# Optimization experiments

Measured on AMD Instinct MI355X. Metric: run time of the kernel, lower is better.

## Reference

```python
import jax, jax.numpy as jnp
import numpy as np

B, L, H, TE = 256, 2048, 64, 64  # batch, seq len, hidden_size, num_time_enc_dims


def _lin_init(k, out_d, in_d):
    bound = 1.0 / np.sqrt(in_d)
    kw, kb = jax.random.split(k)
    w = jax.random.uniform(kw, (out_d, in_d), jnp.float32, -bound, bound)
    b = jax.random.uniform(kb, (out_d,), jnp.float32, -bound, bound)
    return w, b


def setup_inputs() -> dict:
    key = jax.random.key(0)
    ks = jax.random.split(key, 16)
    x_xy = jax.random.normal(ks[0], (B, L, 2), jnp.float32)
    mask = jax.random.bernoulli(ks[1], 0.8, (B, L, 1)).astype(jnp.float32)  # 0 => masked position
    x = jnp.concatenate([x_xy, mask], axis=-1)  # (B,L,3)
    t = jax.random.uniform(ks[2], (B, L, 1), jnp.float32)
    te_w1, te_b1 = _lin_init(ks[3], TE, 1)
    te_w2, te_b2 = _lin_init(ks[4], TE, TE)
    fproj_w, fproj_b = _lin_init(ks[5], H, 3 + TE)
    bproj_w, bproj_b = _lin_init(ks[6], H, 3 + TE)
    fwz, fbz = _lin_init(ks[7], H, H)
    fwh, fbh = _lin_init(ks[8], H, H)
    bwz, bbz = _lin_init(ks[9], H, H)
    bwh, bbh = _lin_init(ks[10], H, H)
    head_hidden = max((2 * H + TE) // 2, 128)  # = 128
    gh_w1, gh_b1 = _lin_init(ks[11], head_hidden, 2 * H + TE)
    gh_w2, gh_b2 = _lin_init(ks[12], 1, head_hidden)
    mask_token = jnp.array([0.0, 0.01], jnp.float32) + jnp.array([0.1, 0.001], jnp.float32) * jax.random.normal(ks[13], (2,), jnp.float32)
    return dict(x=x, t=t, mask_token=mask_token,
                te_w1=te_w1, te_b1=te_b1, te_w2=te_w2, te_b2=te_b2,
                fproj_w=fproj_w, fproj_b=fproj_b, bproj_w=bproj_w, bproj_b=bproj_b,
                fwz=fwz, fbz=fbz, fwh=fwh, fbh=fbh,
                bwz=bwz, bbz=bbz, bwh=bwh, bbh=bbh,
                gh_w1=gh_w1, gh_b1=gh_b1, gh_w2=gh_w2, gh_b2=gh_b2)


def _mingru_prestates(inp, wz, bz, wh, bh, reverse):
    # inp: (B,L,H). Returns the hidden state BEFORE each step's update, in
    # time order, matching the torch code which stores h_* before cell.step.
    z = jax.nn.sigmoid(jnp.einsum('blh,oh->blo', inp, wz) + bz)
    h_tilde = jnp.tanh(jnp.einsum('blh,oh->blo', inp, wh) + bh)

    def step(h, zh):
        z_t, ht_t = zh
        return (1.0 - z_t) * h + z_t * ht_t, h  # emit pre-update carry

    h0 = jnp.zeros((inp.shape[0], wz.shape[0]), inp.dtype)
    _, hs = jax.lax.scan(step, h0,
                         (jnp.swapaxes(z, 0, 1), jnp.swapaxes(h_tilde, 0, 1)),
                         reverse=reverse)
    return jnp.swapaxes(hs, 0, 1)  # (B,L,H)


def reference(x, t, mask_token,
              te_w1, te_b1, te_w2, te_b2,
              fproj_w, fproj_b, bproj_w, bproj_b,
              fwz, fbz, fwh, fbh,
              bwz, bbz, bwh, bbh,
              gh_w1, gh_b1, gh_w2, gh_b2):
    mask_chan = x[..., 2:3]                      # (B,L,1)
    masked_pos = mask_chan == 0
    x_first2 = jnp.where(masked_pos, mask_token.reshape(1, 1, 2), x[..., :2])
    x3 = jnp.concatenate([x_first2, mask_chan], axis=-1)  # (B,L,3)

    t_enc = jax.nn.relu(jnp.einsum('blk,ok->blo', t, te_w1) + te_b1)
    t_enc = jnp.einsum('blk,ok->blo', t_enc, te_w2) + te_b2  # (B,L,TE)

    x_cat = jnp.concatenate([x3, t_enc], axis=-1)  # (B,L,3+TE)

    inp_fwd = jnp.einsum('blk,ok->blo', x_cat, fproj_w) + fproj_b
    inp_bwd = jnp.einsum('blk,ok->blo', x_cat, bproj_w) + bproj_b

    h_fwd = _mingru_prestates(inp_fwd, fwz, fbz, fwh, fbh, reverse=False)  # state after steps 0..t-1
    h_bwd = _mingru_prestates(inp_bwd, bwz, bbz, bwh, bbh, reverse=True)   # state after steps L-1..t+1

    h_fwd_final = h_fwd[:, -1:, :]  # state after steps 0..L-2
    h_bwd_final = h_bwd[:, 0:1, :]  # state after steps L-1..1

    unmasked = mask_chan > 0
    h_fwd_apply = jnp.where(unmasked, h_fwd, h_fwd_final)
    h_bwd_apply = jnp.where(unmasked, h_bwd, h_bwd_final)

    h_bi = jnp.concatenate([h_fwd_apply, h_bwd_apply, t_enc], axis=-1)  # (B,L,2H+TE)
    hid = jax.nn.relu(jnp.einsum('blk,ok->blo', h_bi, gh_w1) + gh_b1)
    preds = jnp.einsum('blk,ok->blo', hid, gh_w2) + gh_b2  # (B,L,1)
    return preds
```

## Files before the change

kernel.cpp:

```cpp
#include <hip/hip_runtime.h>
#include <stdint.h>

#define NB 256
#define NL 2048

typedef __attribute__((ext_vector_type(8))) short short8;
typedef __attribute__((ext_vector_type(4))) float f32x4;
#define MFMA16(a,b,c) __builtin_amdgcn_mfma_f32_16x16x32_bf16(a,b,c,0,0,0)

static __device__ __forceinline__ unsigned short f2bf(float f) {
    union { float f; uint32_t u; } v; v.f = f;
    uint32_t u = v.u;
    uint32_t r = u + 0x7fffu + ((u >> 16) & 1u);
    return (unsigned short)(r >> 16);
}
static __device__ __forceinline__ float bflo(uint32_t u) {
    union { uint32_t u; float f; } v; v.u = u << 16; return v.f;
}
static __device__ __forceinline__ float bfhi(uint32_t u) {
    union { uint32_t u; float f; } v; v.u = u & 0xffff0000u; return v.f;
}
#if __has_builtin(__builtin_amdgcn_cvt_pk_bf16_f32)
typedef __attribute__((ext_vector_type(2))) __bf16 bf16x2_t;
static __device__ __forceinline__ uint32_t pk2(float lo, float hi) {
    union { bf16x2_t v; uint32_t u; } c;
    c.v = __builtin_amdgcn_cvt_pk_bf16_f32(lo, hi);
    return c.u;
}
static __device__ __forceinline__ unsigned short bf1(float v) {
    union { bf16x2_t v; uint32_t u; } c;
    c.v = __builtin_amdgcn_cvt_pk_bf16_f32(v, v);
    return (unsigned short)(c.u & 0xffffu);
}
#else
static __device__ __forceinline__ uint32_t pk2(float lo, float hi) {
    return ((uint32_t)f2bf(hi) << 16) | (uint32_t)f2bf(lo);
}
static __device__ __forceinline__ unsigned short bf1(float v) { return f2bf(v); }
#endif
static __device__ __forceinline__ short8 frag8(const float* p) {
    short8 r;
#pragma unroll
    for (int j = 0; j < 8; ++j) r[j] = (short)f2bf(p[j]);
    return r;
}

static __device__ __forceinline__ void barrier_lds() {
    asm volatile("s_waitcnt lgkmcnt(0)" ::: "memory");
    __builtin_amdgcn_s_barrier();
}

#define SSTR 129

__global__ __launch_bounds__(512) void scan_fused(
    const float* __restrict__ x, const float* __restrict__ t,
    const float* __restrict__ mtok,
    const float* __restrict__ te_w1, const float* __restrict__ te_b1,
    const float* __restrict__ te_w2, const float* __restrict__ te_b2,
    const float* __restrict__ fpw, const float* __restrict__ fpb,
    const float* __restrict__ bpw, const float* __restrict__ bpb,
    const float* __restrict__ fwz, const float* __restrict__ fbz,
    const float* __restrict__ fwh, const float* __restrict__ fbh,
    const float* __restrict__ bwz, const float* __restrict__ bbz,
    const float* __restrict__ bwh, const float* __restrict__ bbh,
    int b0,
    unsigned short* __restrict__ hf, unsigned short* __restrict__ hb)
{
    __shared__ __align__(16) unsigned short s_tenc[128*72];
    __shared__ __align__(16) unsigned short s_inp[128*72];
    __shared__ uint32_t s_seg[64*SSTR];
    __shared__ float s_A[8][65], s_B[8][65];
    __shared__ float s_H[64];
    __shared__ float2 s_wb[64];

    const int rl  = blockIdx.x >> 1;
    const int dir = blockIdx.x & 1;
    const int tid = threadIdx.x;
    const int h   = tid & 63;
    const int q   = tid >> 6;
    const int lq  = h >> 4;
    const int ln  = h & 15;
    const int mq  = q >> 1;
    const int nh  = q & 1;

    const int gx = (b0 + rl) << 11;
    unsigned short* out = (dir ? hb : hf) + (size_t)rl * NL * 64;

    short8 bte[2][2];
    float bite[2];
#pragma unroll
    for (int ni = 0; ni < 2; ++ni) {
        const int nt = nh*2 + ni;
        const float* row = te_w2 + (nt*16 + ln)*64;
#pragma unroll
        for (int ks = 0; ks < 2; ++ks) bte[ni][ks] = frag8(row + lq*8 + ks*32);
        bite[ni] = te_b2[nt*16 + ln];
    }
    const float* PW = dir ? bpw : fpw;
    const float* PB = dir ? bpb : fpb;
    short8 bpj[2][3];
    float bipj[2];
#pragma unroll
    for (int ni = 0; ni < 2; ++ni) {
        const int nt = nh*2 + ni;
        const float* row = PW + (nt*16 + ln)*67;
#pragma unroll
        for (int ks = 0; ks < 2; ++ks) {
            float tmp[8];
#pragma unroll
            for (int j = 0; j < 8; ++j) tmp[j] = row[3 + lq*8 + ks*32 + j];
            bpj[ni][ks] = frag8(tmp);
        }
        {
            float tmp[8];
#pragma unroll
            for (int j = 0; j < 8; ++j) tmp[j] = (lq == 0 && j < 3) ? row[j] : 0.f;
            bpj[ni][2] = frag8(tmp);
        }
        bipj[ni] = PB[nt*16 + ln];
    }
    const float* WZ = dir ? bwz : fwz;
    const float* WH = dir ? bwh : fwh;
    const float* BZ = dir ? bbz : fbz;
    const float* BH = dir ? bbh : fbh;
    short8 bz[2][2], bh[2][2];
    float biz[2], bih[2];
#pragma unroll
    for (int ni = 0; ni < 2; ++ni) {
        const int nt = nh*2 + ni;
        const float* rz = WZ + (nt*16 + ln)*64;
        const float* rh = WH + (nt*16 + ln)*64;
#pragma unroll
        for (int ks = 0; ks < 2; ++ks) {
            bz[ni][ks] = frag8(rz + lq*8 + ks*32);
            bh[ni][ks] = frag8(rh + lq*8 + ks*32);
        }
        biz[ni] = BZ[nt*16 + ln];
        bih[ni] = BH[nt*16 + ln];
    }
    const float mt0 = mtok[0], mt1 = mtok[1];

    auto G1 = [&](const float* tvv) {
#pragma unroll
        for (int mi = 0; mi < 2; ++mi) {
            short8 a0, a1;
#pragma unroll
            for (int j = 0; j < 8; ++j) {
                const float2 wb0 = s_wb[lq*8 + j];
                const float2 wb1 = s_wb[lq*8 + 32 + j];
                a0[j] = (short)bf1(fmaxf(fmaf(tvv[mi], wb0.x, wb0.y), 0.f));
                a1[j] = (short)bf1(fmaxf(fmaf(tvv[mi], wb1.x, wb1.y), 0.f));
            }
#pragma unroll
            for (int ni = 0; ni < 2; ++ni) {
                f32x4 c = {0.f, 0.f, 0.f, 0.f};
                c = MFMA16(a0, bte[ni][0], c);
                c = MFMA16(a1, bte[ni][1], c);
                const int o = (nh*2+ni)*16 + ln;
#pragma unroll
                for (int r = 0; r < 4; ++r)
                    s_tenc[((mq*2+mi)*16 + lq*4 + r)*72 + o] = bf1(c[r] + bite[ni]);
            }
        }
    };
    auto G2 = [&](const float* xr0_, const float* xr1_, const float* xmc_) {
#pragma unroll
        for (int mi = 0; mi < 2; ++mi) {
            const int mrow = (mq*2+mi)*16 + ln;
            const short8 a0 = *(const short8*)(s_tenc + mrow*72 + lq*8);
            const short8 a1 = *(const short8*)(s_tenc + mrow*72 + lq*8 + 32);
            short8 a2 = {0,0,0,0,0,0,0,0};
            if (lq == 0) {
                const float mc  = xmc_[mi];
                const float x0m = (mc == 0.f) ? mt0 : xr0_[mi];
                const float x1m = (mc == 0.f) ? mt1 : xr1_[mi];
                a2[0] = (short)bf1(x0m);
                a2[1] = (short)bf1(x1m);
                a2[2] = (short)bf1(mc);
            }
#pragma unroll
            for (int ni = 0; ni < 2; ++ni) {
                f32x4 c = {0.f, 0.f, 0.f, 0.f};
                c = MFMA16(a0, bpj[ni][0], c);
                c = MFMA16(a1, bpj[ni][1], c);
                c = MFMA16(a2, bpj[ni][2], c);
                const int o = (nh*2+ni)*16 + ln;
#pragma unroll
                for (int r = 0; r < 4; ++r)
                    s_inp[((mq*2+mi)*16 + lq*4 + r)*72 + o] = bf1(c[r] + bipj[ni]);
            }
        }
    };
    auto GATES = [&]() {
#pragma unroll
        for (int mi = 0; mi < 2; ++mi) {
            const int mrow = (mq*2+mi)*16 + ln;
            const short8 a0 = *(const short8*)(s_inp + mrow*72 + lq*8);
            const short8 a1 = *(const short8*)(s_inp + mrow*72 + lq*8 + 32);
#pragma unroll
            for (int ni = 0; ni < 2; ++ni) {
                f32x4 cz  = {0.f, 0.f, 0.f, 0.f};
                f32x4 ch2 = {0.f, 0.f, 0.f, 0.f};
                cz  = MFMA16(a0, bz[ni][0], cz);
                cz  = MFMA16(a1, bz[ni][1], cz);
                ch2 = MFMA16(a0, bh[ni][0], ch2);
                ch2 = MFMA16(a1, bh[ni][1], ch2);
                const int hcol = (nh*2+ni)*16 + ln;
#pragma unroll
                for (int r = 0; r < 4; ++r) {
                    const float az = cz[r]  + biz[ni];
                    const float ah = ch2[r] + bih[ni];
                    const float z  = __builtin_amdgcn_rcpf(1.f + __expf(-az));
                    const float cc = fminf(fmaxf(ah, -15.f), 15.f);
                    const float e2 = __expf(2.f * cc);
                    const float th = 1.f - 2.f * __builtin_amdgcn_rcpf(e2 + 1.f);
                    s_seg[hcol*SSTR + (mq*2+mi)*16 + lq*4 + r] = pk2(1.f - z, z * th);
                }
            }
        }
    };

    if (tid < 64) {
        s_H[tid] = 0.f;
        s_wb[tid] = make_float2(te_w1[tid], te_b1[tid]);
    }
    barrier_lds();

    const int s0 = dir ? 15 : 0;
    {
        float tv0[2];
#pragma unroll
        for (int mi = 0; mi < 2; ++mi)
            tv0[mi] = t[gx + s0*128 + (mq*2+mi)*16 + ln];
        G1(tv0);
    }
    barrier_lds();
    {
        float xr0_[2], xr1_[2], xmc_[2];
        if (lq == 0) {
#pragma unroll
            for (int mi = 0; mi < 2; ++mi) {
                const float* xp = x + (size_t)(gx + s0*128 + (mq*2+mi)*16 + ln)*3;
                xr0_[mi] = xp[0]; xr1_[mi] = xp[1]; xmc_[mi] = xp[2];
            }
        }
        G2(xr0_, xr1_, xmc_);
    }
    barrier_lds();

    uint32_t regs[16];
    int l0p = 0;

#pragma unroll 1
    for (int si = 0; si < 16; ++si) {
        const int s = dir ? (15 - si) : si;
        const int sn = dir ? (14 - si) : (si + 1);
        if (si > 0) {
            float hv = s_A[q][h];
#pragma unroll
            for (int i = 0; i < 16; ++i) {
                const int g = q*16 + i;
                const int xx = dir ? (127 - g) : g;
                out[(size_t)(l0p + xx)*64 + h] = bf1(hv);
                hv = fmaf(bflo(regs[i]), hv, bfhi(regs[i]));
            }
        }
        GATES();
        barrier_lds();
        float tvn[2];
        if (si < 15) {
#pragma unroll
            for (int mi = 0; mi < 2; ++mi)
                tvn[mi] = t[gx + sn*128 + (mq*2+mi)*16 + ln];
        }
        {
            float A = 1.f, Bc = 0.f;
#pragma unroll
            for (int i = 0; i < 16; ++i) {
                const int g = q*16 + i;
                const int xx = dir ? (127 - g) : g;
                const uint32_t uab = s_seg[h*SSTR + xx];
                regs[i] = uab;
                Bc = fmaf(bflo(uab), Bc, bfhi(uab));
                A *= bflo(uab);
            }
            s_A[q][h] = A; s_B[q][h] = Bc;
        }
        if (si < 15) G1(tvn);
        barrier_lds();
        float xr0_[2], xr1_[2], xmc_[2];
        if (si < 15 && lq == 0) {
#pragma unroll
            for (int mi = 0; mi < 2; ++mi) {
                const float* xp = x + (size_t)(gx + sn*128 + (mq*2+mi)*16 + ln)*3;
                xr0_[mi] = xp[0]; xr1_[mi] = xp[1]; xmc_[mi] = xp[2];
            }
        }
        if (tid < 64) {
            float H = s_H[tid];
#pragma unroll
            for (int qq = 0; qq < 8; ++qq) {
                const float a = s_A[qq][tid], b = s_B[qq][tid];
                s_A[qq][tid] = H;
                H = fmaf(a, H, b);
            }
            s_H[tid] = H;
        }
        if (si < 15) G2(xr0_, xr1_, xmc_);
        barrier_lds();
        l0p = s * 128;
    }
    {
        float hv = s_A[q][h];
#pragma unroll
        for (int i = 0; i < 16; ++i) {
            const int g = q*16 + i;
            const int xx = dir ? (127 - g) : g;
            out[(size_t)(l0p + xx)*64 + h] = bf1(hv);
            hv = fmaf(bflo(regs[i]), hv, bfhi(regs[i]));
        }
    }
}

__global__ __launch_bounds__(256, 3) void head_kernel(
    const float* __restrict__ x, const float* __restrict__ t,
    const float* __restrict__ te_w1, const float* __restrict__ te_b1,
    const float* __restrict__ te_w2, const float* __restrict__ te_b2,
    const unsigned short* __restrict__ hf, const unsigned short* __restrict__ hb,
    const float* __restrict__ w1, const float* __restrict__ b1,
    const float* __restrict__ w2, const float* __restrict__ b2,
    int b0,
    float* __restrict__ out)
{
    __shared__ __align__(16) unsigned short s_a[64*200];
    __shared__ float s_part[4][64];
    __shared__ float s_mcall[256];
    __shared__ float2 s_wb[64];

    const int tid = threadIdx.x;
    const int w   = tid >> 6;
    const int l   = tid & 63;
    const int lq  = l >> 4;
    const int ln  = l & 15;

    short8 bw1[2][6];
    float b1v[2], w2v[2];
#pragma unroll
    for (int p = 0; p < 2; ++p) {
        const int o = (2*w + p)*16 + ln;
        const float* row = w1 + o*192;
#pragma unroll
        for (int ks = 0; ks < 6; ++ks) bw1[p][ks] = frag8(row + lq*8 + ks*32);
        b1v[p] = b1[o];
        w2v[p] = w2[o];
    }
    short8 bte[2];
    {
        const float* row = te_w2 + (w*16 + ln)*64;
#pragma unroll
        for (int ks = 0; ks < 2; ++ks) bte[ks] = frag8(row + lq*8 + ks*32);
    }
    const float bias_te = te_b2[w*16 + ln];
    const float bias2 = b2[0];

    const int baseposl = blockIdx.x * 256;
    const int gbase0 = (b0 << 11) + baseposl;

    uint4 greg[4];

    auto GISSUE = [&](int ch) {
        const int chbase = baseposl + ch*64;
        const int ll0 = chbase & 2047;
        const int bl  = chbase >> 11;
        const size_t rowbase = (size_t)bl * NL * 64;
#pragma unroll
        for (int rep = 0; rep < 4; ++rep) {
            const int idx = rep*256 + tid;
            const int seg = idx >> 9;
            const int row = (idx >> 3) & 63;
            const int c   = idx & 7;
            const bool unm = s_mcall[ch*64 + row] > 0.f;
            const uint4* src = (seg == 0)
                ? (const uint4*)(hf + rowbase + (size_t)(unm ? (ll0+row) : (NL-1))*64)
                : (const uint4*)(hb + rowbase + (size_t)(unm ? (ll0+row) : 0)*64);
            greg[rep] = src[c];
        }
    };
    auto GWRITE = [&]() {
#pragma unroll
        for (int rep = 0; rep < 4; ++rep) {
            const int idx = rep*256 + tid;
            const int seg = idx >> 9;
            const int row = (idx >> 3) & 63;
            const int c   = idx & 7;
            ((uint4*)s_a)[row*25 + seg*8 + c] = greg[rep];
        }
    };
    auto TENC = [&](int ch) {
        const int chbase = gbase0 + ch*64;
        const int o = w*16 + ln;
#pragma unroll
        for (int mt = 0; mt < 4; ++mt) {
            const float tv = t[chbase + mt*16 + ln];
            short8 a0, a1;
#pragma unroll
            for (int j = 0; j < 8; ++j) {
                const float2 wb0 = s_wb[lq*8 + j];
                const float2 wb1 = s_wb[lq*8 + 32 + j];
                a0[j] = (short)bf1(fmaxf(fmaf(tv, wb0.x, wb0.y), 0.f));
                a1[j] = (short)bf1(fmaxf(fmaf(tv, wb1.x, wb1.y), 0.f));
            }
            f32x4 c = {0.f, 0.f, 0.f, 0.f};
            c = MFMA16(a0, bte[0], c);
            c = MFMA16(a1, bte[1], c);
#pragma unroll
            for (int r = 0; r < 4; ++r)
                s_a[(mt*16 + lq*4 + r)*200 + 128 + o] = bf1(c[r] + bias_te);
        }
    };
    auto Cp = [&]() {
#pragma unroll
        for (int mt = 0; mt < 4; ++mt) {
            short8 af[6];
#pragma unroll
            for (int ks = 0; ks < 6; ++ks)
                af[ks] = *(const short8*)(s_a + (mt*16+ln)*200 + lq*8 + ks*32);
            float vs[4] = {0.f, 0.f, 0.f, 0.f};
#pragma unroll
            for (int p = 0; p < 2; ++p) {
                f32x4 c = {0.f, 0.f, 0.f, 0.f};
#pragma unroll
                for (int ks = 0; ks < 6; ++ks) c = MFMA16(af[ks], bw1[p][ks], c);
#pragma unroll
                for (int r = 0; r < 4; ++r)
                    vs[r] += fmaxf(c[r] + b1v[p], 0.f) * w2v[p];
            }
#pragma unroll
            for (int mask = 1; mask < 16; mask <<= 1) {
#pragma unroll
                for (int r = 0; r < 4; ++r)
                    vs[r] += __shfl_xor(vs[r], mask);
            }
            if (ln == 0) {
#pragma unroll
                for (int r = 0; r < 4; ++r)
                    s_part[w][mt*16 + lq*4 + r] = vs[r];
            }
        }
    };
    auto Dp = [&](int ch) {
        if (tid < 64) {
            out[gbase0 + ch*64 + tid] = s_part[0][tid] + s_part[1][tid]
                                      + s_part[2][tid] + s_part[3][tid] + bias2;
        }
    };

    s_mcall[tid] = x[(size_t)(gbase0 + tid)*3 + 2];
    if (tid < 64) s_wb[tid] = make_float2(te_w1[tid], te_b1[tid]);
    barrier_lds();
    GISSUE(0);

#pragma unroll 1
    for (int ch = 0; ch < 4; ++ch) {
        if (ch > 0) Dp(ch - 1);
        TENC(ch);
        GWRITE();
        barrier_lds();
        if (ch < 3) GISSUE(ch + 1);
        Cp();
        barrier_lds();
    }
    Dp(3);
}

extern "C" void kernel_launch(void* const* d_in, const int* in_sizes, int n_in,
                              void* d_out, int out_size, void* d_ws, size_t ws_size,
                              hipStream_t stream)
{
    const float* x     = (const float*)d_in[0];
    const float* t     = (const float*)d_in[1];
    const float* mtok  = (const float*)d_in[2];
    const float* te_w1 = (const float*)d_in[3];
    const float* te_b1 = (const float*)d_in[4];
    const float* te_w2 = (const float*)d_in[5];
    const float* te_b2 = (const float*)d_in[6];
    const float* fpw   = (const float*)d_in[7];
    const float* fpb   = (const float*)d_in[8];
    const float* bpw   = (const float*)d_in[9];
    const float* bpb   = (const float*)d_in[10];
    const float* fwz   = (const float*)d_in[11];
    const float* fbz   = (const float*)d_in[12];
    const float* fwh   = (const float*)d_in[13];
    const float* fbh   = (const float*)d_in[14];
    const float* bwz   = (const float*)d_in[15];
    const float* bbz   = (const float*)d_in[16];
    const float* bwh   = (const float*)d_in[17];
    const float* bbh   = (const float*)d_in[18];
    const float* w1    = (const float*)d_in[19];
    const float* b1    = (const float*)d_in[20];
    const float* w2    = (const float*)d_in[21];
    const float* b2    = (const float*)d_in[22];

    const size_t per_b = 524288ull;
    int Bg = NB;
    while ((size_t)Bg * per_b > ws_size && Bg > 1) Bg >>= 1;
    const int nG = NB / Bg;

    char* ws = (char*)d_ws;
    unsigned short* hf = (unsigned short*)ws;
    unsigned short* hb = hf + (size_t)Bg * NL * 64;

    for (int g = 0; g < nG; ++g) {
        const int b0 = g * Bg;

        scan_fused<<<2 * Bg, 512, 0, stream>>>(
            x, t, mtok, te_w1, te_b1, te_w2, te_b2,
            fpw, fpb, bpw, bpb, fwz, fbz, fwh, fbh, bwz, bbz, bwh, bbh,
            b0, hf, hb);

        head_kernel<<<8 * Bg, 256, 0, stream>>>(
            x, t, te_w1, te_b1, te_w2, te_b2,
            hf, hb, w1, b1, w2, b2, b0, (float*)d_out);
    }
}
```

Before: 336.3 us.

## Load GRU state fragments directly from global into MFMA operands in head kernel

The head kernel no longer stages forward and backward hidden states through LDS in four pipelined chunks. It computes the time encoding for all 256 rows up front into a smaller LDS buffer, then each wave loads its hf/hb MFMA A-fragments straight from global memory. The aim is to remove the LDS round trip and most of the barriers. In exchange it drops the explicit prefetch overlap, and each wave now redundantly re-reads the same hf/hb rows from global or cache.

```diff
diff --git a/kernel.cpp b/kernel.cpp
--- a/kernel.cpp
+++ b/kernel.cpp
@@ -332,8 +332,8 @@
     int b0,
     float* __restrict__ out)
 {
-    __shared__ __align__(16) unsigned short s_a[64*200];
-    __shared__ float s_part[4][64];
+    __shared__ __align__(16) unsigned short s_tenc[256*72];
+    __shared__ float s_part[4][256];
     __shared__ float s_mcall[256];
     __shared__ float2 s_wb[64];
 
@@ -365,43 +365,19 @@
 
     const int baseposl = blockIdx.x * 256;
     const int gbase0 = (b0 << 11) + baseposl;
-
-    uint4 greg[4];
-
-    auto GISSUE = [&](int ch) {
-        const int chbase = baseposl + ch*64;
-        const int ll0 = chbase & 2047;
-        const int bl  = chbase >> 11;
-        const size_t rowbase = (size_t)bl * NL * 64;
-#pragma unroll
-        for (int rep = 0; rep < 4; ++rep) {
-            const int idx = rep*256 + tid;
-            const int seg = idx >> 9;
-            const int row = (idx >> 3) & 63;
-            const int c   = idx & 7;
-            const bool unm = s_mcall[ch*64 + row] > 0.f;
-            const uint4* src = (seg == 0)
-                ? (const uint4*)(hf + rowbase + (size_t)(unm ? (ll0+row) : (NL-1))*64)
-                : (const uint4*)(hb + rowbase + (size_t)(unm ? (ll0+row) : 0)*64);
-            greg[rep] = src[c];
-        }
-    };
-    auto GWRITE = [&]() {
-#pragma unroll
-        for (int rep = 0; rep < 4; ++rep) {
-            const int idx = rep*256 + tid;
-            const int seg = idx >> 9;
-            const int row = (idx >> 3) & 63;
-            const int c   = idx & 7;
-            ((uint4*)s_a)[row*25 + seg*8 + c] = greg[rep];
-        }
-    };
-    auto TENC = [&](int ch) {
-        const int chbase = gbase0 + ch*64;
+    const int ll0 = baseposl & 2047;
+    const int bl  = baseposl >> 11;
+    const size_t rowbase = (size_t)bl * NL * 64;
+
+    s_mcall[tid] = x[(size_t)(gbase0 + tid)*3 + 2];
+    if (tid < 64) s_wb[tid] = make_float2(te_w1[tid], te_b1[tid]);
+    barrier_lds();
+
+    {
         const int o = w*16 + ln;
-#pragma unroll
-        for (int mt = 0; mt < 4; ++mt) {
-            const float tv = t[chbase + mt*16 + ln];
+#pragma unroll 2
+        for (int mt = 0; mt < 16; ++mt) {
+            const float tv = t[gbase0 + mt*16 + ln];
             short8 a0, a1;
 #pragma unroll
             for (int j = 0; j < 8; ++j) {
@@ -415,62 +391,52 @@
             c = MFMA16(a1, bte[1], c);
 #pragma unroll
             for (int r = 0; r < 4; ++r)
-                s_a[(mt*16 + lq*4 + r)*200 + 128 + o] = bf1(c[r] + bias_te);
-        }
-    };
-    auto Cp = [&]() {
-#pragma unroll
-        for (int mt = 0; mt < 4; ++mt) {
-            short8 af[6];
-#pragma unroll
-            for (int ks = 0; ks < 6; ++ks)
-                af[ks] = *(const short8*)(s_a + (mt*16+ln)*200 + lq*8 + ks*32);
-            float vs[4] = {0.f, 0.f, 0.f, 0.f};
-#pragma unroll
-            for (int p = 0; p < 2; ++p) {
-                f32x4 c = {0.f, 0.f, 0.f, 0.f};
-#pragma unroll
-                for (int ks = 0; ks < 6; ++ks) c = MFMA16(af[ks], bw1[p][ks], c);
-#pragma unroll
-                for (int r = 0; r < 4; ++r)
-                    vs[r] += fmaxf(c[r] + b1v[p], 0.f) * w2v[p];
-            }
-#pragma unroll
-            for (int mask = 1; mask < 16; mask <<= 1) {
-#pragma unroll
-                for (int r = 0; r < 4; ++r)
-                    vs[r] += __shfl_xor(vs[r], mask);
-            }
-            if (ln == 0) {
-#pragma unroll
-                for (int r = 0; r < 4; ++r)
-                    s_part[w][mt*16 + lq*4 + r] = vs[r];
-            }
-        }
-    };
-    auto Dp = [&](int ch) {
-        if (tid < 64) {
-            out[gbase0 + ch*64 + tid] = s_part[0][tid] + s_part[1][tid]
-                                      + s_part[2][tid] + s_part[3][tid] + bias2;
-        }
-    };
-
-    s_mcall[tid] = x[(size_t)(gbase0 + tid)*3 + 2];
-    if (tid < 64) s_wb[tid] = make_float2(te_w1[tid], te_b1[tid]);
-    barrier_lds();
-    GISSUE(0);
-
-#pragma unroll 1
-    for (int ch = 0; ch < 4; ++ch) {
-        if (ch > 0) Dp(ch - 1);
-        TENC(ch);
-        GWRITE();
-        barrier_lds();
-        if (ch < 3) GISSUE(ch + 1);
-        Cp();
-        barrier_lds();
-    }
-    Dp(3);
+                s_tenc[(mt*16 + lq*4 + r)*72 + o] = bf1(c[r] + bias_te);
+        }
+    }
+    barrier_lds();
+
+#pragma unroll 2
+    for (int mt = 0; mt < 16; ++mt) {
+        const int row = mt*16 + ln;
+        const bool unm = s_mcall[row] > 0.f;
+        const unsigned short* rf = hf + rowbase
+            + (size_t)(unm ? (ll0 + row) : (NL - 1)) * 64;
+        const unsigned short* rb = hb + rowbase
+            + (size_t)(unm ? (ll0 + row) : 0) * 64;
+        short8 af[6];
+        af[0] = *(const short8*)(rf + lq*8);
+        af[1] = *(const short8*)(rf + lq*8 + 32);
+        af[2] = *(const short8*)(rb + lq*8);
+        af[3] = *(const short8*)(rb + lq*8 + 32);
+        af[4] = *(const short8*)(s_tenc + row*72 + lq*8);
+        af[5] = *(const short8*)(s_tenc + row*72 + lq*8 + 32);
+        float vs[4] = {0.f, 0.f, 0.f, 0.f};
+#pragma unroll
+        for (int p = 0; p < 2; ++p) {
+            f32x4 c = {0.f, 0.f, 0.f, 0.f};
+#pragma unroll
+            for (int ks = 0; ks < 6; ++ks) c = MFMA16(af[ks], bw1[p][ks], c);
+#pragma unroll
+            for (int r = 0; r < 4; ++r)
+                vs[r] += fmaxf(c[r] + b1v[p], 0.f) * w2v[p];
+        }
+#pragma unroll
+        for (int mask = 1; mask < 16; mask <<= 1) {
+#pragma unroll
+            for (int r = 0; r < 4; ++r)
+                vs[r] += __shfl_xor(vs[r], mask);
+        }
+        if (ln == 0) {
+#pragma unroll
+            for (int r = 0; r < 4; ++r)
+                s_part[w][mt*16 + lq*4 + r] = vs[r];
+        }
+    }
+    barrier_lds();
+
+    out[gbase0 + tid] = s_part[0][tid] + s_part[1][tid]
+                      + s_part[2][tid] + s_part[3][tid] + bias2;
 }
 
 extern "C" void kernel_launch(void* const* d_in, const int* in_sizes, int n_in,
```

New measurement: 360.4 us. +7.2%, slower.
